# Kernel optimization log

Hardware: AMD Instinct MI355X
Metric: run time of the kernel (lower is better)

Reference implementation:

```python
import jax, jax.numpy as jnp
import numpy as np

B, H, W, C = 128, 56, 56, 96
N = H * W  # tokens


def setup_inputs() -> dict:
    key = jax.random.key(0)
    k1, k2 = jax.random.split(key)
    x = jax.random.normal(k1, (B, N, C), dtype=jnp.float32)
    # original inits to 0.02 * ones; use small random values for a non-trivial baseline
    weight_c = jax.random.uniform(k2, (N, C // 2 + 1, 2), dtype=jnp.float32) * 0.02
    return {"x": x, "weight_c": weight_c}


def reference(x, weight_c):
    # x: [B, N, C]; rfft along channel dim, per-token complex filter, irfft back
    c = x.shape[2]
    xf = jnp.fft.rfft(x.astype(jnp.float32), axis=2, norm="ortho")  # [B, N, C//2+1] complex
    w = jax.lax.complex(weight_c[..., 0], weight_c[..., 1])          # [N, C//2+1] complex
    y = xf * w  # broadcast over batch
    return jnp.fft.irfft(y, n=c, axis=2, norm="ortho")  # [B, N, C]
```

## Files before the change

kernel.cpp:

```cpp
#include <hip/hip_runtime.h>
#include <hip/hip_bf16.h>

#ifndef M_PI
#define M_PI 3.14159265358979323846
#endif

static constexpr int B_ = 128;
static constexpr int N_ = 3136;
static constexpr int C_ = 96;

__global__ __launch_bounds__(192) void gfilter_conv_kernel(
    const float* __restrict__ x, const float* __restrict__ wc,
    float* __restrict__ y) {
  const int n = blockIdx.x;
  const int tid = threadIdx.x;

  __shared__ float At[96 * 132];
  __shared__ float hrep[192];
  __shared__ float wsh[98];
  __shared__ float cs[96];
  __shared__ float sn[96];

  if (tid < 98) wsh[tid] = wc[n * 98 + tid];
  if (tid < 96) {
    float s, c;
    sincosf((float)(2.0 * M_PI / 96.0) * (float)tid, &s, &c);
    cs[tid] = c;
    sn[tid] = s;
  }

  for (int p = 0; p < 16; ++p) {
    const int fidx = p * 192 + tid;
    const int b = fidx / 24;
    const int t4 = fidx - b * 24;
    const float4 v = *reinterpret_cast<const float4*>(
        x + ((size_t)b * N_ + n) * C_ + 4 * t4);
    const int col = 4 * ((b >> 2) ^ (t4 & 7)) + (b & 3);
    float vv[4] = {v.x, v.y, v.z, v.w};
#pragma unroll
    for (int i = 0; i < 4; ++i) {
      At[(4 * t4 + i) * 132 + col] = vv[i];
    }
  }
  __syncthreads();

  if (tid < 96) {
    const int c = tid;
    float acc = wsh[0] + ((c & 1) ? -wsh[96] : wsh[96]);
    int idx = c;
    for (int k = 1; k <= 47; ++k) {
      acc += 2.0f * (wsh[2 * k] * cs[idx] - wsh[2 * k + 1] * sn[idx]);
      idx += c;
      if (idx >= 96) idx -= 96;
    }
    const float hv = acc * (1.0f / 96.0f);
    hrep[c] = hv;
    hrep[c + 96] = hv;
  }
  __syncthreads();

  const int tidx = tid % 6;
  const int tidy = tid / 6;
  const int c0 = tidx * 16;

  float acc[4][16];
#pragma unroll
  for (int i = 0; i < 4; ++i)
#pragma unroll
    for (int j = 0; j < 16; ++j) acc[i][j] = 0.0f;

  float w[16];
#pragma unroll
  for (int j = 0; j < 16; ++j) w[j] = hrep[c0 + j];

  const float4* At4 = reinterpret_cast<const float4*>(At);

#pragma unroll 1
  for (int tt = 0; tt < 96; tt += 16) {
#pragma unroll
    for (int s = 0; s < 16; ++s) {
      const int t = tt + s;
      const float4 a = At4[t * 33 + (tidy ^ ((t >> 2) & 7))];
      float av[4] = {a.x, a.y, a.z, a.w};
#pragma unroll
      for (int i = 0; i < 4; ++i)
#pragma unroll
        for (int j = 0; j < 16; ++j)
          acc[i][j] = fmaf(av[i], w[(j - s) & 15], acc[i][j]);
      w[(15 - s) & 15] = hrep[c0 + 95 - t];
    }
  }

  const int b0 = tidy * 4;
#pragma unroll
  for (int i = 0; i < 4; ++i) {
    float* yp = y + ((size_t)(b0 + i) * N_ + n) * C_ + c0;
#pragma unroll
    for (int q = 0; q < 4; ++q) {
      float4 o = make_float4(acc[i][4 * q + 0], acc[i][4 * q + 1],
                             acc[i][4 * q + 2], acc[i][4 * q + 3]);
      *reinterpret_cast<float4*>(yp + 4 * q) = o;
    }
  }
}

extern "C" void kernel_launch(void* const* d_in, const int* in_sizes, int n_in,
                              void* d_out, int out_size, void* d_ws, size_t ws_size,
                              hipStream_t stream) {
  const float* x = (const float*)d_in[0];
  const float* wc = (const float*)d_in[1];
  float* y = (float*)d_out;

  hipLaunchKernelGGL(gfilter_conv_kernel, dim3(N_), dim3(192), 0, stream,
                     x, wc, y);
}
```

Measured before the change: 324.3 us.

## Compute per-token circular convolution with bf16 MFMA on a circulant matrix

Replaces the scalar FMA circular convolution with a matrix multiply on matrix cores. The batch-by-channel tile of x and an explicitly built 96x96 circulant filter matrix are both converted to bf16 and fed to mfma_f32_16x16x32_bf16. Global loads are issued into registers before the filter setup, so they overlap the sincos and DFT work. This cuts ALU work, but rounding inputs and filter to bf16 adds precision loss, and the output stores become scalar, which may reduce store efficiency.

```diff
diff --git a/kernel.cpp b/kernel.cpp
--- a/kernel.cpp
+++ b/kernel.cpp
@@ -8,18 +8,38 @@
 static constexpr int B_ = 128;
 static constexpr int N_ = 3136;
 static constexpr int C_ = 96;
+static constexpr int PITCH = 104;
 
-__global__ __launch_bounds__(192) void gfilter_conv_kernel(
+typedef short short8 __attribute__((ext_vector_type(8)));
+typedef float float4v __attribute__((ext_vector_type(4)));
+
+static __device__ __forceinline__ unsigned short f2bf(float f) {
+  __hip_bfloat16 b = __float2bfloat16(f);
+  return *reinterpret_cast<unsigned short*>(&b);
+}
+
+__global__ __launch_bounds__(256, 3) void gf_mfma_kernel(
     const float* __restrict__ x, const float* __restrict__ wc,
     float* __restrict__ y) {
   const int n = blockIdx.x;
   const int tid = threadIdx.x;
 
-  __shared__ float At[96 * 132];
-  __shared__ float hrep[192];
+  __shared__ __align__(16) unsigned short Asm[128 * PITCH];
+  __shared__ __align__(16) unsigned short Ht[96 * PITCH];
   __shared__ float wsh[98];
   __shared__ float cs[96];
   __shared__ float sn[96];
+  __shared__ unsigned short hrevd[192];
+
+  float4 xv[12];
+  const float* xbase = x + (size_t)n * C_;
+#pragma unroll
+  for (int p = 0; p < 12; ++p) {
+    const int fidx = p * 256 + tid;
+    const int b = fidx / 24;
+    const int t4 = fidx - b * 24;
+    xv[p] = *reinterpret_cast<const float4*>(xbase + (size_t)b * (N_ * C_) + 4 * t4);
+  }
 
   if (tid < 98) wsh[tid] = wc[n * 98 + tid];
   if (tid < 96) {
@@ -27,20 +47,6 @@
     sincosf((float)(2.0 * M_PI / 96.0) * (float)tid, &s, &c);
     cs[tid] = c;
     sn[tid] = s;
-  }
-
-  for (int p = 0; p < 16; ++p) {
-    const int fidx = p * 192 + tid;
-    const int b = fidx / 24;
-    const int t4 = fidx - b * 24;
-    const float4 v = *reinterpret_cast<const float4*>(
-        x + ((size_t)b * N_ + n) * C_ + 4 * t4);
-    const int col = 4 * ((b >> 2) ^ (t4 & 7)) + (b & 3);
-    float vv[4] = {v.x, v.y, v.z, v.w};
-#pragma unroll
-    for (int i = 0; i < 4; ++i) {
-      At[(4 * t4 + i) * 132 + col] = vv[i];
-    }
   }
   __syncthreads();
 
@@ -53,53 +59,77 @@
       idx += c;
       if (idx >= 96) idx -= 96;
     }
-    const float hv = acc * (1.0f / 96.0f);
-    hrep[c] = hv;
-    hrep[c + 96] = hv;
+    const unsigned short hb = f2bf(acc * (1.0f / 96.0f));
+    hrevd[96 - c] = hb;
+    hrevd[(c == 0) ? 0 : (192 - c)] = hb;
+  }
+
+#pragma unroll
+  for (int p = 0; p < 12; ++p) {
+    const int fidx = p * 256 + tid;
+    const int b = fidx / 24;
+    const int t4 = fidx - b * 24;
+    ushort4 o;
+    o.x = f2bf(xv[p].x);
+    o.y = f2bf(xv[p].y);
+    o.z = f2bf(xv[p].z);
+    o.w = f2bf(xv[p].w);
+    *reinterpret_cast<ushort4*>(&Asm[b * PITCH + 4 * t4]) = o;
   }
   __syncthreads();
 
-  const int tidx = tid % 6;
-  const int tidy = tid / 6;
-  const int c0 = tidx * 16;
+  for (int j = tid; j < 96 * 48; j += 256) {
+    const int c = j / 48;
+    const int kp = j - c * 48;
+    const int m = 96 - c + 2 * kp;
+    const unsigned int lo = hrevd[m];
+    const unsigned int hi = hrevd[m + 1];
+    *reinterpret_cast<unsigned int*>(&Ht[c * PITCH + 2 * kp]) = lo | (hi << 16);
+  }
+  __syncthreads();
 
-  float acc[4][16];
+  const int wv = tid >> 6;
+  const int l = tid & 63;
+  const int lrow = l & 15;
+  const int lk = l >> 4;
+
+  float4v acc[2][6];
 #pragma unroll
-  for (int i = 0; i < 4; ++i)
+  for (int mt = 0; mt < 2; ++mt)
 #pragma unroll
-    for (int j = 0; j < 16; ++j) acc[i][j] = 0.0f;
+    for (int nt = 0; nt < 6; ++nt)
+#pragma unroll
+      for (int i = 0; i < 4; ++i) acc[mt][nt][i] = 0.0f;
 
-  float w[16];
+  short8 afr[2][3];
 #pragma unroll
-  for (int j = 0; j < 16; ++j) w[j] = hrep[c0 + j];
+  for (int mt = 0; mt < 2; ++mt)
+#pragma unroll
+    for (int kq = 0; kq < 3; ++kq)
+      afr[mt][kq] = *reinterpret_cast<const short8*>(
+          &Asm[((wv * 2 + mt) * 16 + lrow) * PITCH + kq * 32 + lk * 8]);
 
-  const float4* At4 = reinterpret_cast<const float4*>(At);
-
-#pragma unroll 1
-  for (int tt = 0; tt < 96; tt += 16) {
 #pragma unroll
-    for (int s = 0; s < 16; ++s) {
-      const int t = tt + s;
-      const float4 a = At4[t * 33 + (tidy ^ ((t >> 2) & 7))];
-      float av[4] = {a.x, a.y, a.z, a.w};
+  for (int nt = 0; nt < 6; ++nt) {
 #pragma unroll
-      for (int i = 0; i < 4; ++i)
-#pragma unroll
-        for (int j = 0; j < 16; ++j)
-          acc[i][j] = fmaf(av[i], w[(j - s) & 15], acc[i][j]);
-      w[(15 - s) & 15] = hrep[c0 + 95 - t];
+    for (int kq = 0; kq < 3; ++kq) {
+      const short8 bfr = *reinterpret_cast<const short8*>(
+          &Ht[(nt * 16 + lrow) * PITCH + kq * 32 + lk * 8]);
+      acc[0][nt] = __builtin_amdgcn_mfma_f32_16x16x32_bf16(afr[0][kq], bfr, acc[0][nt], 0, 0, 0);
+      acc[1][nt] = __builtin_amdgcn_mfma_f32_16x16x32_bf16(afr[1][kq], bfr, acc[1][nt], 0, 0, 0);
     }
   }
 
-  const int b0 = tidy * 4;
 #pragma unroll
-  for (int i = 0; i < 4; ++i) {
-    float* yp = y + ((size_t)(b0 + i) * N_ + n) * C_ + c0;
+  for (int mt = 0; mt < 2; ++mt) {
+    const int brow0 = (wv * 2 + mt) * 16 + lk * 4;
 #pragma unroll
-    for (int q = 0; q < 4; ++q) {
-      float4 o = make_float4(acc[i][4 * q + 0], acc[i][4 * q + 1],
-                             acc[i][4 * q + 2], acc[i][4 * q + 3]);
-      *reinterpret_cast<float4*>(yp + 4 * q) = o;
+    for (int i = 0; i < 4; ++i) {
+      float* yp = y + (size_t)(brow0 + i) * (N_ * C_) + (size_t)n * C_;
+#pragma unroll
+      for (int nt = 0; nt < 6; ++nt) {
+        yp[nt * 16 + lrow] = acc[mt][nt][i];
+      }
     }
   }
 }
@@ -111,6 +141,5 @@
   const float* wc = (const float*)d_in[1];
   float* y = (float*)d_out;
 
-  hipLaunchKernelGGL(gfilter_conv_kernel, dim3(N_), dim3(192), 0, stream,
-                     x, wc, y);
+  hipLaunchKernelGGL(gf_mfma_kernel, dim3(N_), dim3(256), 0, stream, x, wc, y);
 }
```

After: 284.7 us. 12.2% less time.
